# Performance work log

Hardware: AMD Instinct MI355X
Metric: run time of the kernel (lower is better)

Reference implementation:

```python
import jax, jax.numpy as jnp
import numpy as np

H = 4            # heads
C = 64           # per-head dim (= hidden, PyG TransformerConv semantics)
HD = 64          # hidden_dim
L = 2            # num_layers
NT = 2           # node types: 0=task, 1=machine
ET = ((0, 1), (1, 0))  # edge types: (src_nt, dst_nt)
N = 16384        # nodes per type (== max_nodes -> simple pos-enc slice)
E = 262144       # edges per edge type


def _ln(x, g, b):
    mu = x.mean(-1, keepdims=True)
    var = ((x - mu) ** 2).mean(-1, keepdims=True)
    return (x - mu) * jax.lax.rsqrt(var + 1e-5) * g + b


def _tconv(x_src, x_dst, ei, Wq, bq, Wk, bk, Wv, bv, Ws, bs, Wb):
    # PyG TransformerConv: heads=H, out_channels=C, concat=False, beta=True
    n_dst = x_dst.shape[0]
    src, dst = ei[0], ei[1]
    q = (x_dst @ Wq + bq).reshape(-1, H, C)
    k = (x_src @ Wk + bk).reshape(-1, H, C)
    v = (x_src @ Wv + bv).reshape(-1, H, C)
    logits = jnp.einsum('ehc,ehc->eh', q[dst], k[src]) * (1.0 / float(np.sqrt(C)))  # [E,H]
    m = jax.ops.segment_max(logits, dst, num_segments=n_dst)          # [N,H] segment softmax
    ex = jnp.exp(logits - m[dst])
    denom = jax.ops.segment_sum(ex, dst, num_segments=n_dst)
    alpha = ex / denom[dst]                                            # [E,H]
    msg = (alpha[:, :, None] * v[src]).reshape(-1, H * C)              # [E,H*C]
    out = jax.ops.segment_sum(msg, dst, num_segments=n_dst)
    out = out.reshape(n_dst, H, C).mean(axis=1)                        # concat=False -> head mean
    r = x_dst @ Ws + bs                                                # lin_skip
    beta = jax.nn.sigmoid(jnp.concatenate([out, r, out - r], -1) @ Wb) # lin_beta, [N,1]
    return beta * r + (1.0 - beta) * out


def _forward(edge_index, x, W_in, b_in, type_emb, pos, Wq, bq, Wk, bk, Wv, bv,
             Wskip, bskip, Wbeta, ln_g, ln_b, ff_W1, ff_b1, ff_W2, ff_b2, W_out, b_out):
    # input proj + type embedding + positional encoding (num_nodes == max_nodes -> slice)
    h = [x[t] @ W_in[t] + b_in[t] + type_emb[t] + pos[t] for t in range(NT)]
    for l in range(L):
        hn = [jnp.zeros_like(h[0]), jnp.zeros_like(h[1])]
        for e, (s, d) in enumerate(ET):  # HeteroConv, aggr='sum'
            hn[d] = hn[d] + _tconv(h[s], h[d], edge_index[e],
                                   Wq[l, e], bq[l, e], Wk[l, e], bk[l, e],
                                   Wv[l, e], bv[l, e], Wskip[l, e], bskip[l, e], Wbeta[l, e])
        for t in range(NT):
            hr = _ln(h[t] + hn[t], ln_g[l, t], ln_b[l, t])
            ff = jax.nn.gelu(hr @ ff_W1[l, t] + ff_b1[l, t], approximate=False) @ ff_W2[l, t] + ff_b2[l, t]
            h[t] = hr + ff
    return jnp.stack([h[t] @ W_out[t] + b_out[t] for t in range(NT)])  # [NT,N,HD]


def setup_inputs() -> dict:
    key = jax.random.key(0)
    ks = jax.random.split(key, 16)
    w = lambda k, s: 0.02 * jax.random.normal(k, s, jnp.float32)
    NE = len(ET)
    return {
        'x': jax.random.normal(ks[0], (NT, N, HD), jnp.float32),
        'edge_index': jax.random.randint(ks[1], (NE, 2, E), 0, N, jnp.int32),
        'W_in': w(ks[2], (NT, HD, HD)), 'b_in': jnp.zeros((NT, HD), jnp.float32),
        'type_emb': w(ks[3], (NT, HD)),
        'pos': w(ks[4], (NT, N, HD)),
        'Wq': w(ks[5], (L, NE, HD, H * C)), 'bq': jnp.zeros((L, NE, H * C), jnp.float32),
        'Wk': w(ks[6], (L, NE, HD, H * C)), 'bk': jnp.zeros((L, NE, H * C), jnp.float32),
        'Wv': w(ks[7], (L, NE, HD, H * C)), 'bv': jnp.zeros((L, NE, H * C), jnp.float32),
        'Wskip': w(ks[8], (L, NE, HD, HD)), 'bskip': jnp.zeros((L, NE, HD), jnp.float32),
        'Wbeta': w(ks[9], (L, NE, 3 * HD, 1)),
        'ln_g': jnp.ones((L, NT, HD), jnp.float32), 'ln_b': jnp.zeros((L, NT, HD), jnp.float32),
        'ff_W1': w(ks[10], (L, NT, HD, 4 * HD)), 'ff_b1': jnp.zeros((L, NT, 4 * HD), jnp.float32),
        'ff_W2': w(ks[11], (L, NT, 4 * HD, HD)), 'ff_b2': jnp.zeros((L, NT, HD), jnp.float32),
        'W_out': w(ks[12], (NT, HD, HD)), 'b_out': jnp.zeros((NT, HD), jnp.float32),
    }


def reference(x, edge_index, W_in, b_in, type_emb, pos, Wq, bq, Wk, bk, Wv, bv,
              Wskip, bskip, Wbeta, ln_g, ln_b, ff_W1, ff_b1, ff_W2, ff_b2, W_out, b_out):
    return _forward(edge_index, x, W_in, b_in, type_emb, pos, Wq, bq, Wk, bk, Wv, bv,
                    Wskip, bskip, Wbeta, ln_g, ln_b, ff_W1, ff_b1, ff_W2, ff_b2, W_out, b_out)
```

## Files before the change

kernel.cpp:

```cpp
#include <hip/hip_runtime.h>
#include <math.h>

#define NN 16384
#define EE 262144

typedef __bf16 v8bf __attribute__((ext_vector_type(8)));
typedef __bf16 v4bf __attribute__((ext_vector_type(4)));
typedef float  v4f  __attribute__((ext_vector_type(4)));
typedef float  v2f  __attribute__((ext_vector_type(2)));

#define OFF_CNT     0
#define OFF_FILL    (2*NN)
#define OFF_ROWPTR  (4*NN)
#define OFF_COLSRC  98816
#define OFF_H       623104
#define OFF_HN      (OFF_H  + 2*NN*64)
#define OFF_Q       (OFF_HN + 2*NN*64)
#define OFF_KV      (OFF_Q  + 2*NN*128)
#define OFF_R       (OFF_KV + 2*NN*128)

__device__ __forceinline__ float blo(unsigned u) { return __uint_as_float(u << 16); }
__device__ __forceinline__ float bhi(unsigned u) { return __uint_as_float(u & 0xffff0000u); }
__device__ __forceinline__ unsigned short f2b(float f) {
  __bf16 h = (__bf16)f;
  return *(unsigned short*)&h;
}

__global__ void count_kernel(const int* __restrict__ ei, int* __restrict__ cnt) {
  int idx = blockIdx.x * 256 + threadIdx.x;
  if (idx >= 2 * EE) return;
  int et = idx >> 18;
  int j  = idx & (EE - 1);
  int dst = ei[et * 2 * EE + EE + j];
  atomicAdd(&cnt[et * NN + dst], 1);
}

__global__ __launch_bounds__(1024) void scan_kernel(const int* __restrict__ cnt,
                                                    int* __restrict__ rowptr,
                                                    int* __restrict__ fill) {
  int et = blockIdx.x;
  const int* c = cnt + et * NN;
  __shared__ int sums[1024];
  int tid = threadIdx.x;
  int base = tid * 16;
  int loc[16];
  int s = 0;
#pragma unroll
  for (int i = 0; i < 16; ++i) { loc[i] = s; s += c[base + i]; }
  sums[tid] = s;
  __syncthreads();
  for (int off = 1; off < 1024; off <<= 1) {
    int v = 0;
    if (tid >= off) v = sums[tid - off];
    __syncthreads();
    if (tid >= off) sums[tid] += v;
    __syncthreads();
  }
  int ebase = (tid == 0) ? 0 : sums[tid - 1];
  int* rp = rowptr + et * (NN + 1);
  int* fl = fill + et * NN;
#pragma unroll
  for (int i = 0; i < 16; ++i) {
    rp[base + i] = ebase + loc[i];
    fl[base + i] = ebase + loc[i];
  }
  if (tid == 1023) rp[NN] = sums[1023];
}

__global__ void scatter_kernel(const int* __restrict__ ei, int* __restrict__ fill,
                               int* __restrict__ colsrc) {
  int idx = blockIdx.x * 256 + threadIdx.x;
  if (idx >= 2 * EE) return;
  int et = idx >> 18;
  int j  = idx & (EE - 1);
  int src = ei[et * 2 * EE + j];
  int dst = ei[et * 2 * EE + EE + j];
  int pos = atomicAdd(&fill[et * NN + dst], 1);
  colsrc[et * EE + pos] = (et * NN + src) << 9;
}

struct GemmDesc {
  const float *A, *B, *bias, *bias2, *add;
  char* C;
  int Ncols, Cld, ntiles, gelu, otype;
};
struct GemmPack { GemmDesc d[8]; int nd; };

#define LDA 72

__global__ __launch_bounds__(256) void gemm_mfma(GemmPack p) {
  GemmDesc g = p.d[blockIdx.y];
  const int row0 = blockIdx.x * 128;
  const int tid = threadIdx.x;
  const int w = tid >> 6, lane = tid & 63;
  const int l16 = lane & 15, quad = lane >> 4;

  __shared__ __bf16 As[128 * LDA];
  __shared__ __bf16 Bs[64 * LDA];

#pragma unroll
  for (int it = 0; it < 8; ++it) {
    int fi = it * 256 + tid;
    int grow = fi >> 4;
    int kq = (fi & 15) << 2;
    float4 a = *(const float4*)(g.A + (size_t)(row0 + grow) * 64 + kq);
    v4bf c = { (__bf16)a.x, (__bf16)a.y, (__bf16)a.z, (__bf16)a.w };
    *(v4bf*)&As[grow * LDA + kq] = c;
  }

  for (int ct0 = 0; ct0 < g.ntiles; ++ct0) {
    const int col0 = ct0 * 64;
    __syncthreads();
#pragma unroll
    for (int it = 0; it < 4; ++it) {
      int fi = it * 256 + tid;
      int kk = fi >> 4;
      int nq = (fi & 15) << 2;
      float4 b = *(const float4*)(g.B + (size_t)kk * g.Ncols + col0 + nq);
      Bs[(nq + 0) * LDA + kk] = (__bf16)b.x;
      Bs[(nq + 1) * LDA + kk] = (__bf16)b.y;
      Bs[(nq + 2) * LDA + kk] = (__bf16)b.z;
      Bs[(nq + 3) * LDA + kk] = (__bf16)b.w;
    }
    __syncthreads();

    v4f acc[2][4];
#pragma unroll
    for (int rt = 0; rt < 2; ++rt)
#pragma unroll
      for (int ct = 0; ct < 4; ++ct)
#pragma unroll
        for (int r = 0; r < 4; ++r) acc[rt][ct][r] = 0.f;

#pragma unroll
    for (int ks = 0; ks < 2; ++ks) {
      v8bf a0 = *(v8bf*)&As[(w * 32 + l16) * LDA + ks * 32 + quad * 8];
      v8bf a1 = *(v8bf*)&As[(w * 32 + 16 + l16) * LDA + ks * 32 + quad * 8];
#pragma unroll
      for (int ct = 0; ct < 4; ++ct) {
        v8bf bb = *(v8bf*)&Bs[(ct * 16 + l16) * LDA + ks * 32 + quad * 8];
        acc[0][ct] = __builtin_amdgcn_mfma_f32_16x16x32_bf16(a0, bb, acc[0][ct], 0, 0, 0);
        acc[1][ct] = __builtin_amdgcn_mfma_f32_16x16x32_bf16(a1, bb, acc[1][ct], 0, 0, 0);
      }
    }

    float bias_c[4];
#pragma unroll
    for (int ct = 0; ct < 4; ++ct) {
      int col = col0 + ct * 16 + l16;
      float b = g.bias ? g.bias[col] : 0.f;
      if (g.bias2) b += g.bias2[col];
      bias_c[ct] = b;
    }
#pragma unroll
    for (int rt = 0; rt < 2; ++rt)
#pragma unroll
      for (int r = 0; r < 4; ++r) {
        size_t row = row0 + w * 32 + rt * 16 + quad * 4 + r;
        char* cp = g.C + row * (size_t)g.Cld;
#pragma unroll
        for (int ct = 0; ct < 4; ++ct) {
          int col = col0 + ct * 16 + l16;
          float v = acc[rt][ct][r] + bias_c[ct];
          if (g.add) v += g.add[row * g.Ncols + col];
          if (g.gelu) v = 0.5f * v * (1.f + erff(v * 0.70710678118654752f));
          if (g.otype == 0)      *(float*)(cp + col * 4) = v;
          else if (g.otype == 1) *(unsigned short*)(cp + col * 2) = f2b(v);
          else {
            unsigned pk = __builtin_amdgcn_cvt_pk_fp8_f32(v, v, 0, false);
            int boff = ((col >> 3) << 4) + (col & 7) + ((g.otype == 3) ? 8 : 0);
            *(unsigned char*)(cp + boff) = (unsigned char)(pk & 0xff);
          }
        }
      }
  }
}

struct FFPack {
  const float *HN, *W1, *b1, *W2, *b2;
  float* H;
  const float *Wout, *bout;
  float* outbuf;
};

__global__ __launch_bounds__(256) void ff_fused(FFPack p) {
  const int t = blockIdx.y;
  const int row0 = blockIdx.x * 64;
  const int tid = threadIdx.x;
  const int w = tid >> 6, lane = tid & 63;
  const int l16 = lane & 15, quad = lane >> 4;

  const float* A  = p.HN + ((size_t)t * NN) * 64;
  const float* W1 = p.W1 + (size_t)t * 64 * 256;
  const float* b1 = p.b1 + t * 256;
  const float* W2 = p.W2 + (size_t)t * 256 * 64;
  const float* b2 = p.b2 + t * 64;

  __shared__ __bf16 As[64 * LDA];
  __shared__ __bf16 A2[64 * LDA];
  __shared__ __bf16 B1s[64 * LDA];
  __shared__ __bf16 B2s[64 * LDA];

#pragma unroll
  for (int it = 0; it < 4; ++it) {
    int fi = it * 256 + tid;
    int grow = fi >> 4;
    int kq = (fi & 15) << 2;
    float4 a = *(const float4*)(A + (size_t)(row0 + grow) * 64 + kq);
    v4bf c = { (__bf16)a.x, (__bf16)a.y, (__bf16)a.z, (__bf16)a.w };
    *(v4bf*)&As[grow * LDA + kq] = c;
  }

  v4f acc2[4];
#pragma unroll
  for (int ct = 0; ct < 4; ++ct)
#pragma unroll
    for (int r = 0; r < 4; ++r) acc2[ct][r] = 0.f;

  for (int c1 = 0; c1 < 4; ++c1) {
#pragma unroll
    for (int it = 0; it < 4; ++it) {
      int fi = it * 256 + tid;
      int kk = fi >> 4;
      int nq = (fi & 15) << 2;
      float4 b = *(const float4*)(W1 + (size_t)kk * 256 + c1 * 64 + nq);
      B1s[(nq + 0) * LDA + kk] = (__bf16)b.x;
      B1s[(nq + 1) * LDA + kk] = (__bf16)b.y;
      B1s[(nq + 2) * LDA + kk] = (__bf16)b.z;
      B1s[(nq + 3) * LDA + kk] = (__bf16)b.w;
      float4 b2v = *(const float4*)(W2 + (size_t)(c1 * 64 + kk) * 64 + nq);
      B2s[(nq + 0) * LDA + kk] = (__bf16)b2v.x;
      B2s[(nq + 1) * LDA + kk] = (__bf16)b2v.y;
      B2s[(nq + 2) * LDA + kk] = (__bf16)b2v.z;
      B2s[(nq + 3) * LDA + kk] = (__bf16)b2v.w;
    }
    __syncthreads();

    v4f acc1[4];
#pragma unroll
    for (int ct = 0; ct < 4; ++ct)
#pragma unroll
      for (int r = 0; r < 4; ++r) acc1[ct][r] = 0.f;
#pragma unroll
    for (int ks = 0; ks < 2; ++ks) {
      v8bf a = *(v8bf*)&As[(w * 16 + l16) * LDA + ks * 32 + quad * 8];
#pragma unroll
      for (int ct = 0; ct < 4; ++ct) {
        v8bf bb = *(v8bf*)&B1s[(ct * 16 + l16) * LDA + ks * 32 + quad * 8];
        acc1[ct] = __builtin_amdgcn_mfma_f32_16x16x32_bf16(a, bb, acc1[ct], 0, 0, 0);
      }
    }
#pragma unroll
    for (int ct = 0; ct < 4; ++ct) {
      float bb = b1[c1 * 64 + ct * 16 + l16];
#pragma unroll
      for (int r = 0; r < 4; ++r) {
        float v = acc1[ct][r] + bb;
        v = 0.5f * v * (1.f + erff(v * 0.70710678118654752f));
        A2[(w * 16 + quad * 4 + r) * LDA + ct * 16 + l16] = (__bf16)v;
      }
    }
#pragma unroll
    for (int ks = 0; ks < 2; ++ks) {
      v8bf a = *(v8bf*)&A2[(w * 16 + l16) * LDA + ks * 32 + quad * 8];
#pragma unroll
      for (int ct = 0; ct < 4; ++ct) {
        v8bf bb = *(v8bf*)&B2s[(ct * 16 + l16) * LDA + ks * 32 + quad * 8];
        acc2[ct] = __builtin_amdgcn_mfma_f32_16x16x32_bf16(a, bb, acc2[ct], 0, 0, 0);
      }
    }
    __syncthreads();
  }

  if (!p.outbuf) {
#pragma unroll
    for (int ct = 0; ct < 4; ++ct) {
      int col = ct * 16 + l16;
      float bb = b2[col];
#pragma unroll
      for (int r = 0; r < 4; ++r) {
        size_t row = (size_t)t * NN + row0 + w * 16 + quad * 4 + r;
        float v = acc2[ct][r] + bb + p.HN[row * 64 + col];
        p.H[row * 64 + col] = v;
      }
    }
    return;
  }

#pragma unroll
  for (int ct = 0; ct < 4; ++ct) {
    int col = ct * 16 + l16;
    float bb = b2[col];
#pragma unroll
    for (int r = 0; r < 4; ++r) {
      int lrow = w * 16 + quad * 4 + r;
      size_t row = (size_t)t * NN + row0 + lrow;
      float v = acc2[ct][r] + bb + p.HN[row * 64 + col];
      A2[lrow * LDA + col] = (__bf16)v;
    }
  }
  {
    const float* Wo = p.Wout + (size_t)t * 64 * 64;
#pragma unroll
    for (int it = 0; it < 4; ++it) {
      int fi = it * 256 + tid;
      int kk = fi >> 4;
      int nq = (fi & 15) << 2;
      float4 b = *(const float4*)(Wo + (size_t)kk * 64 + nq);
      B1s[(nq + 0) * LDA + kk] = (__bf16)b.x;
      B1s[(nq + 1) * LDA + kk] = (__bf16)b.y;
      B1s[(nq + 2) * LDA + kk] = (__bf16)b.z;
      B1s[(nq + 3) * LDA + kk] = (__bf16)b.w;
    }
  }
  __syncthreads();

  v4f acc3[4];
#pragma unroll
  for (int ct = 0; ct < 4; ++ct)
#pragma unroll
    for (int r = 0; r < 4; ++r) acc3[ct][r] = 0.f;
#pragma unroll
  for (int ks = 0; ks < 2; ++ks) {
    v8bf a = *(v8bf*)&A2[(w * 16 + l16) * LDA + ks * 32 + quad * 8];
#pragma unroll
    for (int ct = 0; ct < 4; ++ct) {
      v8bf bb = *(v8bf*)&B1s[(ct * 16 + l16) * LDA + ks * 32 + quad * 8];
      acc3[ct] = __builtin_amdgcn_mfma_f32_16x16x32_bf16(a, bb, acc3[ct], 0, 0, 0);
    }
  }
  const float* bo = p.bout + t * 64;
#pragma unroll
  for (int ct = 0; ct < 4; ++ct) {
    int col = ct * 16 + l16;
    float bb = bo[col];
#pragma unroll
    for (int r = 0; r < 4; ++r) {
      size_t row = (size_t)t * NN + row0 + w * 16 + quad * 4 + r;
      p.outbuf[row * 64 + col] = acc3[ct][r] + bb;
    }
  }
}

struct AggPack {
  const unsigned short *Q;
  const char *KV;
  const float *R;
  const float *Wb;
  const float *Hin;
  const float *lng, *lnb;
  float* outHR;
  const int *rowptr;
  const int *colsrc;
};

__global__ __launch_bounds__(256) void agg_kernel(AggPack p) {
  const int et = blockIdx.y, d = 1 - et;
  int wid = __builtin_amdgcn_readfirstlane(threadIdx.x >> 6);
  int lane = threadIdx.x & 63;
  int node = blockIdx.x * 4 + wid;
  int lh = lane & 31;
  int half = lane >> 5;

  const int* rp = p.rowptr + et * (NN + 1);
  const int* cs = p.colsrc + et * EE;
  int start = rp[node], end = rp[node + 1];
  int len = end - start;
  int gnode = d * NN + node;

  uint4 qw = *(const uint4*)(p.Q + ((size_t)gnode << 8) + lh * 8);
  float q0 = blo(qw.x) * 0.125f, q1 = bhi(qw.x) * 0.125f;
  float q2 = blo(qw.y) * 0.125f, q3 = bhi(qw.y) * 0.125f;
  float q4 = blo(qw.z) * 0.125f, q5 = bhi(qw.z) * 0.125f;
  float q6 = blo(qw.w) * 0.125f, q7 = bhi(qw.w) * 0.125f;

  int mid = start + (len >> 1);
  int last = end - 1;
  float dsum0 = 0.f, dsum1 = 0.f;
  float acc0[8], acc1[8];
#pragma unroll
  for (int i = 0; i < 8; ++i) { acc0[i] = 0.f; acc1[i] = 0.f; }

  int maxn = (len + 3) >> 2;
  int j0 = start + half, j1 = mid + half;
  bool a0 = j0 < mid, a1 = j1 < end;
  int o0 = 0, o1 = 0;
  if (len > 0) {
    o0 = cs[a0 ? j0 : last];
    o1 = cs[a1 ? j1 : last];
  }
  int lb = lh * 16;
  for (int it = 0; it < maxn; ++it) {
    uint4 kv0 = *(const uint4*)(p.KV + (size_t)(o0 + lb));
    uint4 kv1 = *(const uint4*)(p.KV + (size_t)(o1 + lb));
    float w0 = a0 ? 1.f : 0.f;
    float w1 = a1 ? 1.f : 0.f;
    j0 += 2; j1 += 2;
    a0 = j0 < mid; a1 = j1 < end;
    o0 = cs[a0 ? j0 : last];
    o1 = cs[a1 ? j1 : last];

    {
      v2f ka = __builtin_amdgcn_cvt_pk_f32_fp8((int)kv0.x, false);
      v2f kb = __builtin_amdgcn_cvt_pk_f32_fp8((int)kv0.x, true);
      v2f kc = __builtin_amdgcn_cvt_pk_f32_fp8((int)kv0.y, false);
      v2f kd = __builtin_amdgcn_cvt_pk_f32_fp8((int)kv0.y, true);
      float pd = q0 * ka[0] + q1 * ka[1] + q2 * kb[0] + q3 * kb[1]
               + q4 * kc[0] + q5 * kc[1] + q6 * kd[0] + q7 * kd[1];
      pd += __shfl_xor(pd, 1);
      pd += __shfl_xor(pd, 2);
      pd += __shfl_xor(pd, 4);
      float wgt = w0 * __expf(pd);
      v2f va = __builtin_amdgcn_cvt_pk_f32_fp8((int)kv0.z, false);
      v2f vb = __builtin_amdgcn_cvt_pk_f32_fp8((int)kv0.z, true);
      v2f vc = __builtin_amdgcn_cvt_pk_f32_fp8((int)kv0.w, false);
      v2f vd = __builtin_amdgcn_cvt_pk_f32_fp8((int)kv0.w, true);
      dsum0 += wgt;
      acc0[0] += wgt * va[0]; acc0[1] += wgt * va[1];
      acc0[2] += wgt * vb[0]; acc0[3] += wgt * vb[1];
      acc0[4] += wgt * vc[0]; acc0[5] += wgt * vc[1];
      acc0[6] += wgt * vd[0]; acc0[7] += wgt * vd[1];
    }
    {
      v2f ka = __builtin_amdgcn_cvt_pk_f32_fp8((int)kv1.x, false);
      v2f kb = __builtin_amdgcn_cvt_pk_f32_fp8((int)kv1.x, true);
      v2f kc = __builtin_amdgcn_cvt_pk_f32_fp8((int)kv1.y, false);
      v2f kd = __builtin_amdgcn_cvt_pk_f32_fp8((int)kv1.y, true);
      float pd = q0 * ka[0] + q1 * ka[1] + q2 * kb[0] + q3 * kb[1]
               + q4 * kc[0] + q5 * kc[1] + q6 * kd[0] + q7 * kd[1];
      pd += __shfl_xor(pd, 1);
      pd += __shfl_xor(pd, 2);
      pd += __shfl_xor(pd, 4);
      float wgt = w1 * __expf(pd);
      v2f va = __builtin_amdgcn_cvt_pk_f32_fp8((int)kv1.z, false);
      v2f vb = __builtin_amdgcn_cvt_pk_f32_fp8((int)kv1.z, true);
      v2f vc = __builtin_amdgcn_cvt_pk_f32_fp8((int)kv1.w, false);
      v2f vd = __builtin_amdgcn_cvt_pk_f32_fp8((int)kv1.w, true);
      dsum1 += wgt;
      acc1[0] += wgt * va[0]; acc1[1] += wgt * va[1];
      acc1[2] += wgt * vb[0]; acc1[3] += wgt * vb[1];
      acc1[4] += wgt * vc[0]; acc1[5] += wgt * vc[1];
      acc1[6] += wgt * vd[0]; acc1[7] += wgt * vd[1];
    }
  }

  float dn = dsum0 + dsum1;
  dn += __shfl_xor(dn, 32);
  float inv = (len > 0) ? (0.25f / dn) : 0.f;

  float o_[8];
#pragma unroll
  for (int i = 0; i < 8; ++i) {
    float a = acc0[i] + acc1[i];
    a += __shfl_xor(a, 32);
    a *= inv;
    a += __shfl_xor(a, 8);
    a += __shfl_xor(a, 16);
    o_[i] = a;
  }

  int cc = (lane & 7) << 3;
  const float* rptr = p.R + (size_t)gnode * 64 + cc;
  float4 r0 = *(const float4*)(rptr);
  float4 r1 = *(const float4*)(rptr + 4);
  float rr[8] = { r0.x, r0.y, r0.z, r0.w, r1.x, r1.y, r1.z, r1.w };

  const float* wb = p.Wb + et * 192;
  float4 wo0 = *(const float4*)(wb + cc),       wo1 = *(const float4*)(wb + cc + 4);
  float4 wr0 = *(const float4*)(wb + 64 + cc),  wr1 = *(const float4*)(wb + 64 + cc + 4);
  float4 wd0 = *(const float4*)(wb + 128 + cc), wd1 = *(const float4*)(wb + 128 + cc + 4);
  float wov[8] = { wo0.x, wo0.y, wo0.z, wo0.w, wo1.x, wo1.y, wo1.z, wo1.w };
  float wrv[8] = { wr0.x, wr0.y, wr0.z, wr0.w, wr1.x, wr1.y, wr1.z, wr1.w };
  float wdv[8] = { wd0.x, wd0.y, wd0.z, wd0.w, wd1.x, wd1.y, wd1.z, wd1.w };
  float part = 0.f;
#pragma unroll
  for (int i = 0; i < 8; ++i)
    part += o_[i] * wov[i] + rr[i] * wrv[i] + (o_[i] - rr[i]) * wdv[i];
  part += __shfl_xor(part, 1);
  part += __shfl_xor(part, 2);
  part += __shfl_xor(part, 4);
  float beta = 1.f / (1.f + __expf(-part));

  const float* hptr = p.Hin + (size_t)gnode * 64 + cc;
  float4 h0 = *(const float4*)(hptr);
  float4 h1 = *(const float4*)(hptr + 4);
  float hh[8] = { h0.x, h0.y, h0.z, h0.w, h1.x, h1.y, h1.z, h1.w };
  float y[8];
  float sa = 0.f, sb = 0.f;
#pragma unroll
  for (int i = 0; i < 8; ++i) {
    float v = hh[i] + beta * rr[i] + (1.f - beta) * o_[i];
    y[i] = v;
    sa += v;
    sb += v * v;
  }
  sa += __shfl_xor(sa, 1); sb += __shfl_xor(sb, 1);
  sa += __shfl_xor(sa, 2); sb += __shfl_xor(sb, 2);
  sa += __shfl_xor(sa, 4); sb += __shfl_xor(sb, 4);
  float mu = sa * (1.f / 64.f);
  float var = sb * (1.f / 64.f) - mu * mu;
  float rs = rsqrtf(var + 1e-5f);

  if (lane < 8) {
    const float* lng = p.lng + d * 64 + cc;
    const float* lnb = p.lnb + d * 64 + cc;
    float4 g0 = *(const float4*)(lng);
    float4 g1 = *(const float4*)(lng + 4);
    float4 bb0 = *(const float4*)(lnb);
    float4 bb1 = *(const float4*)(lnb + 4);
    float4 res0, res1;
    res0.x = (y[0] - mu) * rs * g0.x + bb0.x;
    res0.y = (y[1] - mu) * rs * g0.y + bb0.y;
    res0.z = (y[2] - mu) * rs * g0.z + bb0.z;
    res0.w = (y[3] - mu) * rs * g0.w + bb0.w;
    res1.x = (y[4] - mu) * rs * g1.x + bb1.x;
    res1.y = (y[5] - mu) * rs * g1.y + bb1.y;
    res1.z = (y[6] - mu) * rs * g1.z + bb1.z;
    res1.w = (y[7] - mu) * rs * g1.w + bb1.w;
    float* op = p.outHR + (size_t)gnode * 64 + cc;
    *(float4*)(op) = res0;
    *(float4*)(op + 4) = res1;
  }
}

static void add_desc(GemmPack& p, const float* A, const float* B,
                     const float* bias, const float* bias2, const float* add,
                     void* C, int Nc, int Cld, int gelu, int otype) {
  GemmDesc& g = p.d[p.nd++];
  g.A = A; g.B = B; g.bias = bias; g.bias2 = bias2; g.add = add; g.C = (char*)C;
  g.Ncols = Nc; g.Cld = Cld; g.ntiles = Nc / 64;
  g.gelu = gelu; g.otype = otype;
}

extern "C" void kernel_launch(void* const* d_in, const int* in_sizes, int n_in,
                              void* d_out, int out_size, void* d_ws, size_t ws_size,
                              hipStream_t stream) {
  const float* x        = (const float*)d_in[0];
  const int*   ei       = (const int*)d_in[1];
  const float* W_in     = (const float*)d_in[2];
  const float* b_in     = (const float*)d_in[3];
  const float* type_emb = (const float*)d_in[4];
  const float* pos      = (const float*)d_in[5];
  const float* Wq       = (const float*)d_in[6];
  const float* bq       = (const float*)d_in[7];
  const float* Wk       = (const float*)d_in[8];
  const float* bk       = (const float*)d_in[9];
  const float* Wv       = (const float*)d_in[10];
  const float* bv       = (const float*)d_in[11];
  const float* Wskip    = (const float*)d_in[12];
  const float* bskip    = (const float*)d_in[13];
  const float* Wbeta    = (const float*)d_in[14];
  const float* ln_g     = (const float*)d_in[15];
  const float* ln_b     = (const float*)d_in[16];
  const float* ff_W1    = (const float*)d_in[17];
  const float* ff_b1    = (const float*)d_in[18];
  const float* ff_W2    = (const float*)d_in[19];
  const float* ff_b2    = (const float*)d_in[20];
  const float* W_out    = (const float*)d_in[21];
  const float* b_out    = (const float*)d_in[22];
  float* out = (float*)d_out;

  int*   wsi = (int*)d_ws;
  float* wsf = (float*)d_ws;
  int* cnt    = wsi + OFF_CNT;
  int* fill   = wsi + OFF_FILL;
  int* rowptr = wsi + OFF_ROWPTR;
  int* colsrc = wsi + OFF_COLSRC;
  float* H  = wsf + OFF_H;
  float* HN = wsf + OFF_HN;
  unsigned short* Qb = (unsigned short*)(wsf + OFF_Q);
  char* KVb = (char*)(wsf + OFF_KV);
  float* Rb = wsf + OFF_R;

  hipMemsetAsync(cnt, 0, 2 * NN * sizeof(int), stream);
  count_kernel<<<dim3(2 * EE / 256), dim3(256), 0, stream>>>(ei, cnt);
  scan_kernel<<<dim3(2), dim3(1024), 0, stream>>>(cnt, rowptr, fill);
  scatter_kernel<<<dim3(2 * EE / 256), dim3(256), 0, stream>>>(ei, fill, colsrc);

  {
    GemmPack p{};
    for (int t = 0; t < 2; ++t)
      add_desc(p, x + (size_t)t * NN * 64, W_in + t * 64 * 64,
               b_in + t * 64, type_emb + t * 64, pos + (size_t)t * NN * 64,
               H + (size_t)t * NN * 64, 64, 256, 0, 0);
    gemm_mfma<<<dim3(128, p.nd), dim3(256), 0, stream>>>(p);
  }

  for (int l = 0; l < 2; ++l) {
    {
      GemmPack p{};
      for (int et = 0; et < 2; ++et) {
        int s = et, d = 1 - et;
        int we = l * 2 + et;
        const float* hs = H + (size_t)s * NN * 64;
        const float* hd = H + (size_t)d * NN * 64;
        add_desc(p, hd, Wq + (size_t)we * 64 * 256, bq + we * 256,
                 nullptr, nullptr, (char*)Qb + (size_t)d * NN * 512, 256, 512, 0, 1);
        add_desc(p, hs, Wk + (size_t)we * 64 * 256, bk + we * 256,
                 nullptr, nullptr, KVb + (size_t)s * NN * 512, 256, 512, 0, 2);
        add_desc(p, hs, Wv + (size_t)we * 64 * 256, bv + we * 256,
                 nullptr, nullptr, KVb + (size_t)s * NN * 512, 256, 512, 0, 3);
        add_desc(p, hd, Wskip + (size_t)we * 64 * 64, bskip + we * 64,
                 nullptr, nullptr, Rb + (size_t)d * NN * 64, 64, 256, 0, 0);
      }
      gemm_mfma<<<dim3(128, p.nd), dim3(256), 0, stream>>>(p);
    }

    AggPack ap;
    ap.Q = Qb; ap.KV = KVb; ap.R = Rb;
    ap.Wb = Wbeta + l * 2 * 192;
    ap.Hin = H;
    ap.lng = ln_g + l * 128;
    ap.lnb = ln_b + l * 128;
    ap.outHR = HN;
    ap.rowptr = rowptr;
    ap.colsrc = colsrc;
    agg_kernel<<<dim3(NN / 4, 2), dim3(256), 0, stream>>>(ap);

    FFPack fp;
    fp.HN = HN;
    fp.W1 = ff_W1 + (size_t)l * 2 * 64 * 256;
    fp.b1 = ff_b1 + l * 2 * 256;
    fp.W2 = ff_W2 + (size_t)l * 2 * 256 * 64;
    fp.b2 = ff_b2 + l * 2 * 64;
    fp.H  = H;
    fp.Wout = W_out;
    fp.bout = b_out;
    fp.outbuf = (l == 1) ? out : nullptr;
    ff_fused<<<dim3(NN / 64, 2), dim3(256), 0, stream>>>(fp);
  }
}
```

Before: 378.6 us.

## Pre-transpose weights to bf16 once and read MFMA B fragments directly from global

Adds a prep kernel that converts all weight matrices to transposed bf16 once per call. The GEMM and fused FF kernels then load B fragments straight from global memory (L2-resident) and A fragments into registers, instead of staging through LDS with per-block fp32-to-bf16 transposes and __syncthreads. The projection GEMM is regrouped by source node type so one A load feeds Q/K/V/skip tiles spread across waves. The trade-off is an extra kernel launch and global or L2 traffic for B fragments, plus possible load imbalance, since 13 tiles are split over 4 waves.

```diff
diff --git a/kernel.cpp b/kernel.cpp
--- a/kernel.cpp
+++ b/kernel.cpp
@@ -18,12 +18,36 @@
 #define OFF_Q       (OFF_HN + 2*NN*64)
 #define OFF_KV      (OFF_Q  + 2*NN*128)
 #define OFF_R       (OFF_KV + 2*NN*128)
+#define OFF_WT      (OFF_R  + 2*NN*64)
+
+#define WT_Q   0
+#define WT_K   65536
+#define WT_V   131072
+#define WT_S   196608
+#define WT_IN  212992
+#define WT_W1  221184
+#define WT_W2  286720
+#define WT_WO  352256
 
 __device__ __forceinline__ float blo(unsigned u) { return __uint_as_float(u << 16); }
 __device__ __forceinline__ float bhi(unsigned u) { return __uint_as_float(u & 0xffff0000u); }
 __device__ __forceinline__ unsigned short f2b(float f) {
   __bf16 h = (__bf16)f;
   return *(unsigned short*)&h;
+}
+
+struct PrepDesc { const float* src; unsigned short* dst; int ksh; int total; };
+struct PrepPack { PrepDesc d[28]; };
+
+__global__ __launch_bounds__(256) void prep_kernel(PrepPack p) {
+  PrepDesc g = p.d[blockIdx.y];
+  int idx = blockIdx.x * 256 + threadIdx.x;
+  if (idx >= g.total) return;
+  int K = 1 << g.ksh;
+  int n = idx >> g.ksh;
+  int k = idx & (K - 1);
+  int N = g.total >> g.ksh;
+  g.dst[idx] = f2b(g.src[(size_t)k * N + n]);
 }
 
 __global__ void count_kernel(const int* __restrict__ ei, int* __restrict__ cnt) {
@@ -79,50 +103,43 @@
   colsrc[et * EE + pos] = (et * NN + src) << 9;
 }
 
-struct GemmDesc {
-  const float *A, *B, *bias, *bias2, *add;
+struct GDesc {
+  const unsigned short* Bt;
+  const float *bias, *bias2, *add;
   char* C;
-  int Ncols, Cld, ntiles, gelu, otype;
+  int Ncols, Cld, gelu, otype;
 };
-struct GemmPack { GemmDesc d[8]; int nd; };
-
-#define LDA 72
-
-__global__ __launch_bounds__(256) void gemm_mfma(GemmPack p) {
-  GemmDesc g = p.d[blockIdx.y];
-  const int row0 = blockIdx.x * 128;
-  const int tid = threadIdx.x;
-  const int w = tid >> 6, lane = tid & 63;
+struct GGroup {
+  const float* A;
+  GDesc d[4];
+  signed char tdesc[16], tct[16];
+  int ntt;
+};
+struct GPack { GGroup g[2]; };
+
+__global__ __launch_bounds__(256) void gemm_direct(GPack p) {
+  const GGroup& gr = p.g[blockIdx.y];
+  const int row0 = blockIdx.x * 32;
+  const int w = threadIdx.x >> 6, lane = threadIdx.x & 63;
   const int l16 = lane & 15, quad = lane >> 4;
-
-  __shared__ __bf16 As[128 * LDA];
-  __shared__ __bf16 Bs[64 * LDA];
-
-#pragma unroll
-  for (int it = 0; it < 8; ++it) {
-    int fi = it * 256 + tid;
-    int grow = fi >> 4;
-    int kq = (fi & 15) << 2;
-    float4 a = *(const float4*)(g.A + (size_t)(row0 + grow) * 64 + kq);
-    v4bf c = { (__bf16)a.x, (__bf16)a.y, (__bf16)a.z, (__bf16)a.w };
-    *(v4bf*)&As[grow * LDA + kq] = c;
-  }
-
-  for (int ct0 = 0; ct0 < g.ntiles; ++ct0) {
-    const int col0 = ct0 * 64;
-    __syncthreads();
-#pragma unroll
-    for (int it = 0; it < 4; ++it) {
-      int fi = it * 256 + tid;
-      int kk = fi >> 4;
-      int nq = (fi & 15) << 2;
-      float4 b = *(const float4*)(g.B + (size_t)kk * g.Ncols + col0 + nq);
-      Bs[(nq + 0) * LDA + kk] = (__bf16)b.x;
-      Bs[(nq + 1) * LDA + kk] = (__bf16)b.y;
-      Bs[(nq + 2) * LDA + kk] = (__bf16)b.z;
-      Bs[(nq + 3) * LDA + kk] = (__bf16)b.w;
-    }
-    __syncthreads();
+  if (w >= gr.ntt) return;
+
+  v8bf afr[2][2];
+#pragma unroll
+  for (int rt = 0; rt < 2; ++rt)
+#pragma unroll
+    for (int ks = 0; ks < 2; ++ks) {
+      const float* ap = gr.A + (size_t)(row0 + rt * 16 + l16) * 64 + ks * 32 + quad * 8;
+      float4 x0 = *(const float4*)ap;
+      float4 x1 = *(const float4*)(ap + 4);
+      v8bf f = { (__bf16)x0.x, (__bf16)x0.y, (__bf16)x0.z, (__bf16)x0.w,
+                 (__bf16)x1.x, (__bf16)x1.y, (__bf16)x1.z, (__bf16)x1.w };
+      afr[rt][ks] = f;
+    }
+
+  for (int ti = w; ti < gr.ntt; ti += 4) {
+    const GDesc& g = gr.d[gr.tdesc[ti]];
+    const int col0 = gr.tct[ti] * 64;
 
     v4f acc[2][4];
 #pragma unroll
@@ -134,13 +151,11 @@
 
 #pragma unroll
     for (int ks = 0; ks < 2; ++ks) {
-      v8bf a0 = *(v8bf*)&As[(w * 32 + l16) * LDA + ks * 32 + quad * 8];
-      v8bf a1 = *(v8bf*)&As[(w * 32 + 16 + l16) * LDA + ks * 32 + quad * 8];
 #pragma unroll
       for (int ct = 0; ct < 4; ++ct) {
-        v8bf bb = *(v8bf*)&Bs[(ct * 16 + l16) * LDA + ks * 32 + quad * 8];
-        acc[0][ct] = __builtin_amdgcn_mfma_f32_16x16x32_bf16(a0, bb, acc[0][ct], 0, 0, 0);
-        acc[1][ct] = __builtin_amdgcn_mfma_f32_16x16x32_bf16(a1, bb, acc[1][ct], 0, 0, 0);
+        v8bf bb = *(const v8bf*)(g.Bt + (size_t)(col0 + ct * 16 + l16) * 64 + ks * 32 + quad * 8);
+        acc[0][ct] = __builtin_amdgcn_mfma_f32_16x16x32_bf16(afr[0][ks], bb, acc[0][ct], 0, 0, 0);
+        acc[1][ct] = __builtin_amdgcn_mfma_f32_16x16x32_bf16(afr[1][ks], bb, acc[1][ct], 0, 0, 0);
       }
     }
 
@@ -156,7 +171,7 @@
     for (int rt = 0; rt < 2; ++rt)
 #pragma unroll
       for (int r = 0; r < 4; ++r) {
-        size_t row = row0 + w * 32 + rt * 16 + quad * 4 + r;
+        size_t row = row0 + rt * 16 + quad * 4 + r;
         char* cp = g.C + row * (size_t)g.Cld;
 #pragma unroll
         for (int ct = 0; ct < 4; ++ct) {
@@ -176,39 +191,40 @@
   }
 }
 
+#define LDA 72
+
 struct FFPack {
-  const float *HN, *W1, *b1, *W2, *b2;
+  const float *HN;
+  const unsigned short *W1t, *W2t, *Wot;
+  const float *b1, *b2, *bout;
   float* H;
-  const float *Wout, *bout;
   float* outbuf;
 };
 
 __global__ __launch_bounds__(256) void ff_fused(FFPack p) {
   const int t = blockIdx.y;
   const int row0 = blockIdx.x * 64;
-  const int tid = threadIdx.x;
-  const int w = tid >> 6, lane = tid & 63;
+  const int w = threadIdx.x >> 6, lane = threadIdx.x & 63;
   const int l16 = lane & 15, quad = lane >> 4;
+  const int wr = w * 16;
 
   const float* A  = p.HN + ((size_t)t * NN) * 64;
-  const float* W1 = p.W1 + (size_t)t * 64 * 256;
+  const unsigned short* W1t = p.W1t + (size_t)t * 16384;
+  const unsigned short* W2t = p.W2t + (size_t)t * 16384;
   const float* b1 = p.b1 + t * 256;
-  const float* W2 = p.W2 + (size_t)t * 256 * 64;
   const float* b2 = p.b2 + t * 64;
 
-  __shared__ __bf16 As[64 * LDA];
   __shared__ __bf16 A2[64 * LDA];
-  __shared__ __bf16 B1s[64 * LDA];
-  __shared__ __bf16 B2s[64 * LDA];
-
-#pragma unroll
-  for (int it = 0; it < 4; ++it) {
-    int fi = it * 256 + tid;
-    int grow = fi >> 4;
-    int kq = (fi & 15) << 2;
-    float4 a = *(const float4*)(A + (size_t)(row0 + grow) * 64 + kq);
-    v4bf c = { (__bf16)a.x, (__bf16)a.y, (__bf16)a.z, (__bf16)a.w };
-    *(v4bf*)&As[grow * LDA + kq] = c;
+
+  v8bf afr[2];
+#pragma unroll
+  for (int ks = 0; ks < 2; ++ks) {
+    const float* ap = A + (size_t)(row0 + wr + l16) * 64 + ks * 32 + quad * 8;
+    float4 x0 = *(const float4*)ap;
+    float4 x1 = *(const float4*)(ap + 4);
+    v8bf f = { (__bf16)x0.x, (__bf16)x0.y, (__bf16)x0.z, (__bf16)x0.w,
+               (__bf16)x1.x, (__bf16)x1.y, (__bf16)x1.z, (__bf16)x1.w };
+    afr[ks] = f;
   }
 
   v4f acc2[4];
@@ -218,24 +234,6 @@
     for (int r = 0; r < 4; ++r) acc2[ct][r] = 0.f;
 
   for (int c1 = 0; c1 < 4; ++c1) {
-#pragma unroll
-    for (int it = 0; it < 4; ++it) {
-      int fi = it * 256 + tid;
-      int kk = fi >> 4;
-      int nq = (fi & 15) << 2;
-      float4 b = *(const float4*)(W1 + (size_t)kk * 256 + c1 * 64 + nq);
-      B1s[(nq + 0) * LDA + kk] = (__bf16)b.x;
-      B1s[(nq + 1) * LDA + kk] = (__bf16)b.y;
-      B1s[(nq + 2) * LDA + kk] = (__bf16)b.z;
-      B1s[(nq + 3) * LDA + kk] = (__bf16)b.w;
-      float4 b2v = *(const float4*)(W2 + (size_t)(c1 * 64 + kk) * 64 + nq);
-      B2s[(nq + 0) * LDA + kk] = (__bf16)b2v.x;
-      B2s[(nq + 1) * LDA + kk] = (__bf16)b2v.y;
-      B2s[(nq + 2) * LDA + kk] = (__bf16)b2v.z;
-      B2s[(nq + 3) * LDA + kk] = (__bf16)b2v.w;
-    }
-    __syncthreads();
-
     v4f acc1[4];
 #pragma unroll
     for (int ct = 0; ct < 4; ++ct)
@@ -243,11 +241,10 @@
       for (int r = 0; r < 4; ++r) acc1[ct][r] = 0.f;
 #pragma unroll
     for (int ks = 0; ks < 2; ++ks) {
-      v8bf a = *(v8bf*)&As[(w * 16 + l16) * LDA + ks * 32 + quad * 8];
 #pragma unroll
       for (int ct = 0; ct < 4; ++ct) {
-        v8bf bb = *(v8bf*)&B1s[(ct * 16 + l16) * LDA + ks * 32 + quad * 8];
-        acc1[ct] = __builtin_amdgcn_mfma_f32_16x16x32_bf16(a, bb, acc1[ct], 0, 0, 0);
+        v8bf bb = *(const v8bf*)(W1t + (size_t)(c1 * 64 + ct * 16 + l16) * 64 + ks * 32 + quad * 8);
+        acc1[ct] = __builtin_amdgcn_mfma_f32_16x16x32_bf16(afr[ks], bb, acc1[ct], 0, 0, 0);
       }
     }
 #pragma unroll
@@ -257,19 +254,21 @@
       for (int r = 0; r < 4; ++r) {
         float v = acc1[ct][r] + bb;
         v = 0.5f * v * (1.f + erff(v * 0.70710678118654752f));
-        A2[(w * 16 + quad * 4 + r) * LDA + ct * 16 + l16] = (__bf16)v;
+        A2[(wr + quad * 4 + r) * LDA + ct * 16 + l16] = (__bf16)v;
       }
     }
+    v8bf a2fr[2];
+#pragma unroll
+    for (int ks = 0; ks < 2; ++ks)
+      a2fr[ks] = *(v8bf*)&A2[(wr + l16) * LDA + ks * 32 + quad * 8];
 #pragma unroll
     for (int ks = 0; ks < 2; ++ks) {
-      v8bf a = *(v8bf*)&A2[(w * 16 + l16) * LDA + ks * 32 + quad * 8];
 #pragma unroll
       for (int ct = 0; ct < 4; ++ct) {
-        v8bf bb = *(v8bf*)&B2s[(ct * 16 + l16) * LDA + ks * 32 + quad * 8];
-        acc2[ct] = __builtin_amdgcn_mfma_f32_16x16x32_bf16(a, bb, acc2[ct], 0, 0, 0);
+        v8bf bb = *(const v8bf*)(W2t + (size_t)(ct * 16 + l16) * 256 + c1 * 64 + ks * 32 + quad * 8);
+        acc2[ct] = __builtin_amdgcn_mfma_f32_16x16x32_bf16(a2fr[ks], bb, acc2[ct], 0, 0, 0);
       }
     }
-    __syncthreads();
   }
 
   if (!p.outbuf) {
@@ -279,7 +278,7 @@
       float bb = b2[col];
 #pragma unroll
       for (int r = 0; r < 4; ++r) {
-        size_t row = (size_t)t * NN + row0 + w * 16 + quad * 4 + r;
+        size_t row = (size_t)t * NN + row0 + wr + quad * 4 + r;
         float v = acc2[ct][r] + bb + p.HN[row * 64 + col];
         p.H[row * 64 + col] = v;
       }
@@ -293,28 +292,18 @@
     float bb = b2[col];
 #pragma unroll
     for (int r = 0; r < 4; ++r) {
-      int lrow = w * 16 + quad * 4 + r;
+      int lrow = wr + quad * 4 + r;
       size_t row = (size_t)t * NN + row0 + lrow;
       float v = acc2[ct][r] + bb + p.HN[row * 64 + col];
       A2[lrow * LDA + col] = (__bf16)v;
     }
   }
-  {
-    const float* Wo = p.Wout + (size_t)t * 64 * 64;
-#pragma unroll
-    for (int it = 0; it < 4; ++it) {
-      int fi = it * 256 + tid;
-      int kk = fi >> 4;
-      int nq = (fi & 15) << 2;
-      float4 b = *(const float4*)(Wo + (size_t)kk * 64 + nq);
-      B1s[(nq + 0) * LDA + kk] = (__bf16)b.x;
-      B1s[(nq + 1) * LDA + kk] = (__bf16)b.y;
-      B1s[(nq + 2) * LDA + kk] = (__bf16)b.z;
-      B1s[(nq + 3) * LDA + kk] = (__bf16)b.w;
-    }
-  }
-  __syncthreads();
-
+  v8bf a3fr[2];
+#pragma unroll
+  for (int ks = 0; ks < 2; ++ks)
+    a3fr[ks] = *(v8bf*)&A2[(wr + l16) * LDA + ks * 32 + quad * 8];
+
+  const unsigned short* Wot = p.Wot + (size_t)t * 4096;
   v4f acc3[4];
 #pragma unroll
   for (int ct = 0; ct < 4; ++ct)
@@ -322,11 +311,10 @@
     for (int r = 0; r < 4; ++r) acc3[ct][r] = 0.f;
 #pragma unroll
   for (int ks = 0; ks < 2; ++ks) {
-    v8bf a = *(v8bf*)&A2[(w * 16 + l16) * LDA + ks * 32 + quad * 8];
 #pragma unroll
     for (int ct = 0; ct < 4; ++ct) {
-      v8bf bb = *(v8bf*)&B1s[(ct * 16 + l16) * LDA + ks * 32 + quad * 8];
-      acc3[ct] = __builtin_amdgcn_mfma_f32_16x16x32_bf16(a, bb, acc3[ct], 0, 0, 0);
+      v8bf bb = *(const v8bf*)(Wot + (size_t)(ct * 16 + l16) * 64 + ks * 32 + quad * 8);
+      acc3[ct] = __builtin_amdgcn_mfma_f32_16x16x32_bf16(a3fr[ks], bb, acc3[ct], 0, 0, 0);
     }
   }
   const float* bo = p.bout + t * 64;
@@ -336,7 +324,7 @@
     float bb = bo[col];
 #pragma unroll
     for (int r = 0; r < 4; ++r) {
-      size_t row = (size_t)t * NN + row0 + w * 16 + quad * 4 + r;
+      size_t row = (size_t)t * NN + row0 + wr + quad * 4 + r;
       p.outbuf[row * 64 + col] = acc3[ct][r] + bb;
     }
   }
@@ -523,13 +511,11 @@
   }
 }
 
-static void add_desc(GemmPack& p, const float* A, const float* B,
-                     const float* bias, const float* bias2, const float* add,
-                     void* C, int Nc, int Cld, int gelu, int otype) {
-  GemmDesc& g = p.d[p.nd++];
-  g.A = A; g.B = B; g.bias = bias; g.bias2 = bias2; g.add = add; g.C = (char*)C;
-  g.Ncols = Nc; g.Cld = Cld; g.ntiles = Nc / 64;
-  g.gelu = gelu; g.otype = otype;
+static void set_desc(GDesc& g, const unsigned short* Bt, const float* bias,
+                     const float* bias2, const float* add, void* C,
+                     int Nc, int Cld, int gelu, int otype) {
+  g.Bt = Bt; g.bias = bias; g.bias2 = bias2; g.add = add; g.C = (char*)C;
+  g.Ncols = Nc; g.Cld = Cld; g.gelu = gelu; g.otype = otype;
 }
 
 extern "C" void kernel_launch(void* const* d_in, const int* in_sizes, int n_in,
@@ -571,6 +557,25 @@
   unsigned short* Qb = (unsigned short*)(wsf + OFF_Q);
   char* KVb = (char*)(wsf + OFF_KV);
   float* Rb = wsf + OFF_R;
+  unsigned short* wt = (unsigned short*)(wsf + OFF_WT);
+
+  {
+    PrepPack pp{};
+    int nd = 0;
+    for (int we = 0; we < 4; ++we) {
+      pp.d[nd++] = { Wq + (size_t)we * 16384, wt + WT_Q + we * 16384, 6, 16384 };
+      pp.d[nd++] = { Wk + (size_t)we * 16384, wt + WT_K + we * 16384, 6, 16384 };
+      pp.d[nd++] = { Wv + (size_t)we * 16384, wt + WT_V + we * 16384, 6, 16384 };
+      pp.d[nd++] = { Wskip + (size_t)we * 4096, wt + WT_S + we * 4096, 6, 4096 };
+      pp.d[nd++] = { ff_W1 + (size_t)we * 16384, wt + WT_W1 + we * 16384, 6, 16384 };
+      pp.d[nd++] = { ff_W2 + (size_t)we * 16384, wt + WT_W2 + we * 16384, 8, 16384 };
+    }
+    for (int t = 0; t < 2; ++t) {
+      pp.d[nd++] = { W_in + (size_t)t * 4096, wt + WT_IN + t * 4096, 6, 4096 };
+      pp.d[nd++] = { W_out + (size_t)t * 4096, wt + WT_WO + t * 4096, 6, 4096 };
+    }
+    prep_kernel<<<dim3(64, nd), dim3(256), 0, stream>>>(pp);
+  }
 
   hipMemsetAsync(cnt, 0, 2 * NN * sizeof(int), stream);
   count_kernel<<<dim3(2 * EE / 256), dim3(256), 0, stream>>>(ei, cnt);
@@ -578,32 +583,40 @@
   scatter_kernel<<<dim3(2 * EE / 256), dim3(256), 0, stream>>>(ei, fill, colsrc);
 
   {
-    GemmPack p{};
-    for (int t = 0; t < 2; ++t)
-      add_desc(p, x + (size_t)t * NN * 64, W_in + t * 64 * 64,
-               b_in + t * 64, type_emb + t * 64, pos + (size_t)t * NN * 64,
-               H + (size_t)t * NN * 64, 64, 256, 0, 0);
-    gemm_mfma<<<dim3(128, p.nd), dim3(256), 0, stream>>>(p);
+    GPack p{};
+    for (int t = 0; t < 2; ++t) {
+      GGroup& g = p.g[t];
+      g.A = x + (size_t)t * NN * 64;
+      set_desc(g.d[0], wt + WT_IN + t * 4096, b_in + t * 64, type_emb + t * 64,
+               pos + (size_t)t * NN * 64, H + (size_t)t * NN * 64, 64, 256, 0, 0);
+      g.tdesc[0] = 0; g.tct[0] = 0; g.ntt = 1;
+    }
+    gemm_direct<<<dim3(NN / 32, 2), dim3(256), 0, stream>>>(p);
   }
 
   for (int l = 0; l < 2; ++l) {
     {
-      GemmPack p{};
-      for (int et = 0; et < 2; ++et) {
-        int s = et, d = 1 - et;
-        int we = l * 2 + et;
-        const float* hs = H + (size_t)s * NN * 64;
-        const float* hd = H + (size_t)d * NN * 64;
-        add_desc(p, hd, Wq + (size_t)we * 64 * 256, bq + we * 256,
-                 nullptr, nullptr, (char*)Qb + (size_t)d * NN * 512, 256, 512, 0, 1);
-        add_desc(p, hs, Wk + (size_t)we * 64 * 256, bk + we * 256,
-                 nullptr, nullptr, KVb + (size_t)s * NN * 512, 256, 512, 0, 2);
-        add_desc(p, hs, Wv + (size_t)we * 64 * 256, bv + we * 256,
-                 nullptr, nullptr, KVb + (size_t)s * NN * 512, 256, 512, 0, 3);
-        add_desc(p, hd, Wskip + (size_t)we * 64 * 64, bskip + we * 64,
-                 nullptr, nullptr, Rb + (size_t)d * NN * 64, 64, 256, 0, 0);
+      GPack p{};
+      for (int tt = 0; tt < 2; ++tt) {
+        GGroup& g = p.g[tt];
+        g.A = H + (size_t)tt * NN * 64;
+        int we_dst = l * 2 + (1 - tt);
+        int we_src = l * 2 + tt;
+        set_desc(g.d[0], wt + WT_Q + we_dst * 16384, bq + we_dst * 256, nullptr, nullptr,
+                 (char*)Qb + (size_t)tt * NN * 512, 256, 512, 0, 1);
+        set_desc(g.d[1], wt + WT_K + we_src * 16384, bk + we_src * 256, nullptr, nullptr,
+                 KVb + (size_t)tt * NN * 512, 256, 512, 0, 2);
+        set_desc(g.d[2], wt + WT_V + we_src * 16384, bv + we_src * 256, nullptr, nullptr,
+                 KVb + (size_t)tt * NN * 512, 256, 512, 0, 3);
+        set_desc(g.d[3], wt + WT_S + we_dst * 4096, bskip + we_dst * 64, nullptr, nullptr,
+                 Rb + (size_t)tt * NN * 64, 64, 256, 0, 0);
+        int ti = 0;
+        for (int dd = 0; dd < 3; ++dd)
+          for (int ct = 0; ct < 4; ++ct) { g.tdesc[ti] = dd; g.tct[ti] = ct; ++ti; }
+        g.tdesc[ti] = 3; g.tct[ti] = 0; ++ti;
+        g.ntt = ti;
       }
-      gemm_mfma<<<dim3(128, p.nd), dim3(256), 0, stream>>>(p);
+      gemm_direct<<<dim3(NN / 32, 2), dim3(256), 0, stream>>>(p);
     }
 
     AggPack ap;
@@ -619,13 +632,13 @@
 
     FFPack fp;
     fp.HN = HN;
-    fp.W1 = ff_W1 + (size_t)l * 2 * 64 * 256;
+    fp.W1t = wt + WT_W1 + l * 2 * 16384;
+    fp.W2t = wt + WT_W2 + l * 2 * 16384;
+    fp.Wot = wt + WT_WO;
     fp.b1 = ff_b1 + l * 2 * 256;
-    fp.W2 = ff_W2 + (size_t)l * 2 * 256 * 64;
     fp.b2 = ff_b2 + l * 2 * 64;
+    fp.bout = b_out;
     fp.H  = H;
-    fp.Wout = W_out;
-    fp.bout = b_out;
     fp.outbuf = (l == 1) ? out : nullptr;
     ff_fused<<<dim3(NN / 64, 2), dim3(256), 0, stream>>>(fp);
   }
```

After: 427.6 us. 1.13x slower.
